# Kernel optimization log

Measured on AMD Instinct MI355X. Metric: run time of the kernel, lower is better.

## Reference

```python
import jax, jax.numpy as jnp
import numpy as np

B, T, DIM, H = 32, 1024, 512, 8
HD = DIM // H
HID = int(DIM * 4.0)
EPS = 1e-6
SCALE = HD ** -0.5


def _ln(t, g, b):
    m = t.mean(-1, keepdims=True)
    var = ((t - m) ** 2).mean(-1, keepdims=True)
    return (t - m) * jax.lax.rsqrt(var + EPS) * g + b


def setup_inputs() -> dict:
    key = jax.random.key(0)
    ks = jax.random.split(key, 10)
    n = lambda k, s: jax.random.normal(k, s, dtype=jnp.float32)
    w = lambda k, s: n(k, s) * 0.02
    z = lambda d: jnp.zeros((d,), dtype=jnp.float32)
    o = lambda d: jnp.ones((d,), dtype=jnp.float32)
    return {
        'x': n(ks[0], (B, T, DIM)),
        'k': n(ks[1], (T, H, B, HD)),
        'v': n(ks[2], (T, H, B, HD)),
        'Wqkv': w(ks[3], (DIM, 3 * DIM)), 'bqkv': z(3 * DIM),
        'Wsa': w(ks[4], (DIM, DIM)), 'bsa': z(DIM),
        'Wq': w(ks[5], (DIM, DIM)), 'bq': z(DIM),
        'Wed': w(ks[6], (DIM, DIM)), 'bed': z(DIM),
        'g1': o(DIM), 'be1': z(DIM),
        'g2': o(DIM), 'be2': z(DIM),
        'g3': o(DIM), 'be3': z(DIM),
        'W1': w(ks[7], (DIM, HID)), 'b1': z(HID),
        'W2': w(ks[8], (HID, DIM)), 'b2': z(DIM),
    }


def _decoder_block(x, k, v, Wqkv, bqkv, Wsa, bsa, Wq, bq, Wed, bed,
                   g1, be1, g2, be2, g3, be3, W1, b1, W2, b2):
    # ---- self-attention (faithful to the original, degenerate einsums) ----
    qkv = x @ Wqkv + bqkv                                        # [B,T,3*DIM]
    qkv = qkv.reshape(B, T, 3, H, HD).transpose(2, 1, 3, 0, 4)   # [3,T,H,B,HD]
    q, sk, sv = qkv[0], qkv[1], qkv[2]
    dp = jnp.einsum('kabc,qdef->qabe', sk, q) * SCALE            # [T,H,B,B]
    scores = jax.nn.softmax(dp, axis=-1)
    wa = jnp.einsum('qabc,kdef->bqaf', scores, sv).reshape(B, T, DIM)
    attn = wa @ Wsa + bsa
    an1 = _ln(attn + x, g1, be1)
    # ---- encoder-decoder attention ----
    qe = (an1 @ Wq + bq).reshape(B, T, H, HD).transpose(1, 2, 0, 3)  # [T,H,B,HD]
    dp2 = jnp.einsum('abkd,abqd->abqk', k, qe) * SCALE           # [T,H,B,B]
    sc2 = jax.nn.softmax(dp2, axis=-1)
    wa2 = jnp.einsum('abts,abse->tabe', sc2, v).reshape(B, T, DIM)
    attn2 = wa2 @ Wed + bed
    an2 = _ln(attn2 + x, g2, be2)
    # ---- MLP (exact GELU, as nn.GELU default) ----
    hmid = jax.nn.gelu(an2 @ W1 + b1, approximate=False)
    z = hmid @ W2 + b2
    return _ln(z + an2, g3, be3)


def reference(x, k, v, Wqkv, bqkv, Wsa, bsa, Wq, bq, Wed, bed,
              g1, be1, g2, be2, g3, be3, W1, b1, W2, b2):
    return _decoder_block(x, k, v, Wqkv, bqkv, Wsa, bsa, Wq, bq, Wed, bed,
                          g1, be1, g2, be2, g3, be3, W1, b1, W2, b2)
```

## Files before the change

kernel.cpp:

```cpp
#include <hip/hip_runtime.h>
#include <hip/hip_bf16.h>
#include <math.h>

#define Bn 32
#define Tn 1024
#define DIMn 512
#define Hn 8
#define HDn 64
#define HIDn 2048
#define Mn 32768

using short8 = __attribute__((ext_vector_type(8))) short;
using half8  = __attribute__((ext_vector_type(8))) _Float16;
using f32x4  = __attribute__((ext_vector_type(4))) float;
typedef unsigned short u16;
typedef unsigned int   u32;

__device__ __forceinline__ u16 f2h(float x) {
  _Float16 h = (_Float16)x;
  return __builtin_bit_cast(u16, h);
}
__device__ __forceinline__ float h2f(u16 u) {
  return (float)__builtin_bit_cast(_Float16, u);
}
__device__ __forceinline__ u32 pack2h(float a, float b) {
  return (u32)f2h(a) | ((u32)f2h(b) << 16);
}
__device__ __forceinline__ void gld16(const void* g, void* l) {
  __builtin_amdgcn_global_load_lds((const __attribute__((address_space(1))) u32*)g,
                                   (__attribute__((address_space(3))) u32*)l, 16, 0, 0);
}
__device__ __forceinline__ float wredsum(float v) {
  #pragma unroll
  for (int d = 1; d < 64; d <<= 1) v += __shfl_xor(v, d, 64);
  return v;
}
__device__ __forceinline__ void hard_barrier() {
  asm volatile("" ::: "memory");
  __builtin_amdgcn_s_barrier();
  asm volatile("" ::: "memory");
}
__device__ __forceinline__ float fast_gelu(float v) {
  const float ax = fabsf(v) * 0.70710678118654752f;
  const float t = 1.0f / (1.0f + 0.3275911f * ax);
  const float p = ((((1.061405429f * t - 1.453152027f) * t) + 1.421413741f) * t - 0.284496736f) * t + 0.254829592f;
  const float y = 1.0f - p * t * __expf(-ax * ax);
  const float erfv = (v >= 0.f) ? y : -y;
  return 0.5f * v * (1.0f + erfv);
}

__global__ __launch_bounds__(256) void colsum1(const float* __restrict__ x, float* __restrict__ part) {
  const int b = blockIdx.x, t = threadIdx.x;
  const float* p = x + (size_t)b * 128 * DIMn;
  float a0 = 0.f, a1 = 0.f;
  for (int r = 0; r < 128; ++r) {
    a0 += p[r * DIMn + t];
    a1 += p[r * DIMn + t + 256];
  }
  part[b * DIMn + t] = a0;
  part[b * DIMn + t + 256] = a1;
}

__global__ __launch_bounds__(256) void colsum2(const float* __restrict__ part, float* __restrict__ xs) {
  const int c = blockIdx.x * 256 + threadIdx.x;
  float a = 0.f;
  for (int b = 0; b < 256; ++b) a += part[b * DIMn + c];
  xs[c] = a;
}

__global__ __launch_bounds__(256) void sv_k(const float* __restrict__ xs, const float* __restrict__ Wqkv,
                                            const float* __restrict__ bqkv, float* __restrict__ SVp) {
  __shared__ float xsh[512];
  __shared__ float red[4][64];
  const int h = blockIdx.x, q = threadIdx.x >> 6, f = threadIdx.x & 63;
  xsh[threadIdx.x] = xs[threadIdx.x];
  xsh[threadIdx.x + 256] = xs[threadIdx.x + 256];
  __syncthreads();
  const int colb = 2 * DIMn + h * HDn + f;
  float acc = 0.f;
  for (int i = q * 128; i < q * 128 + 128; ++i) acc += xsh[i] * Wqkv[(size_t)i * 1536 + colb];
  red[q][f] = acc;
  __syncthreads();
  if (q == 0)
    SVp[h * 64 + f] = red[0][f] + red[1][f] + red[2][f] + red[3][f] + 32768.0f * bqkv[colb];
}

__global__ __launch_bounds__(256) void attnc2_k(const float* __restrict__ SVp, const float* __restrict__ Wsa,
                                                const float* __restrict__ bsa, float* __restrict__ attnc) {
  __shared__ float SVs[64];
  __shared__ float red[4][64];
  const int q = threadIdx.x >> 6, jj = threadIdx.x & 63;
  if (threadIdx.x < 64) {
    float s = 0.f;
    #pragma unroll
    for (int h = 0; h < 8; ++h) s += SVp[h * 64 + threadIdx.x];
    SVs[threadIdx.x] = s;
  }
  __syncthreads();
  const int j = blockIdx.x * 64 + jj;
  float acc = 0.f;
  for (int i = q * 128; i < q * 128 + 128; ++i) acc += SVs[i & 63] * Wsa[(size_t)i * DIMn + j];
  red[q][jj] = acc;
  __syncthreads();
  if (q == 0) attnc[j] = red[0][jj] + red[1][jj] + red[2][jj] + red[3][jj] + bsa[j];
}

__global__ __launch_bounds__(256) void wtrans(const float* __restrict__ W, u16* __restrict__ WT, int K, int N) {
  __shared__ float tile[64][65];
  const int n0 = blockIdx.x * 64, k0 = blockIdx.y * 64;
  const int t = threadIdx.x;
  #pragma unroll
  for (int i = 0; i < 16; ++i) {
    const int fl = i * 256 + t, r = fl >> 6, c = fl & 63;
    tile[r][c] = W[(size_t)(k0 + r) * N + n0 + c];
  }
  __syncthreads();
  #pragma unroll
  for (int i = 0; i < 16; ++i) {
    const int fl = i * 256 + t, r = fl >> 6, c = fl & 63;
    WT[(size_t)(n0 + r) * K + k0 + c] = f2h(tile[c][r]);
  }
}

template <int MODE>
__global__ __launch_bounds__(256) void ln_k(const void* __restrict__ Ap, const void* __restrict__ Bp,
                                            const float* __restrict__ cv, const float* __restrict__ g,
                                            const float* __restrict__ be, void* __restrict__ outp) {
  const int row = blockIdx.x * 4 + (threadIdx.x >> 6);
  const int l = threadIdx.x & 63;
  const size_t base = (size_t)row * DIMn + l * 8;
  float v[8];
  if (MODE == 0 || MODE == 2) {
    const float* a = (const float*)Ap + base;
    float4 x0 = *(const float4*)a;
    float4 x1 = *(const float4*)(a + 4);
    v[0] = x0.x; v[1] = x0.y; v[2] = x0.z; v[3] = x0.w;
    v[4] = x1.x; v[5] = x1.y; v[6] = x1.z; v[7] = x1.w;
  } else {
    short8 s = *(const short8*)((const u16*)Ap + base);
    #pragma unroll
    for (int i = 0; i < 8; ++i) v[i] = h2f((u16)s[i]);
  }
  if (MODE == 0) {
    float4 c0 = *(const float4*)(cv + l * 8);
    float4 c1 = *(const float4*)(cv + l * 8 + 4);
    v[0] += c0.x; v[1] += c0.y; v[2] += c0.z; v[3] += c0.w;
    v[4] += c1.x; v[5] += c1.y; v[6] += c1.z; v[7] += c1.w;
  } else if (MODE == 1) {
    const float* b = (const float*)Bp + base;
    float4 x0 = *(const float4*)b;
    float4 x1 = *(const float4*)(b + 4);
    v[0] += x0.x; v[1] += x0.y; v[2] += x0.z; v[3] += x0.w;
    v[4] += x1.x; v[5] += x1.y; v[6] += x1.z; v[7] += x1.w;
  } else {
    short8 s2 = *(const short8*)((const u16*)Bp + base);
    #pragma unroll
    for (int i = 0; i < 8; ++i) v[i] += h2f((u16)s2[i]);
  }
  float s = 0.f;
  #pragma unroll
  for (int i = 0; i < 8; ++i) s += v[i];
  s = wredsum(s);
  const float mean = s * (1.0f / 512.0f);
  float q = 0.f;
  #pragma unroll
  for (int i = 0; i < 8; ++i) { const float d = v[i] - mean; q += d * d; }
  q = wredsum(q);
  const float rs = rsqrtf(q * (1.0f / 512.0f) + 1e-6f);
  float gg[8], bb[8];
  {
    float4 g0 = *(const float4*)(g + l * 8);
    float4 g1 = *(const float4*)(g + l * 8 + 4);
    float4 b0 = *(const float4*)(be + l * 8);
    float4 b1 = *(const float4*)(be + l * 8 + 4);
    gg[0] = g0.x; gg[1] = g0.y; gg[2] = g0.z; gg[3] = g0.w;
    gg[4] = g1.x; gg[5] = g1.y; gg[6] = g1.z; gg[7] = g1.w;
    bb[0] = b0.x; bb[1] = b0.y; bb[2] = b0.z; bb[3] = b0.w;
    bb[4] = b1.x; bb[5] = b1.y; bb[6] = b1.z; bb[7] = b1.w;
  }
  float y[8];
  #pragma unroll
  for (int i = 0; i < 8; ++i) y[i] = (v[i] - mean) * rs * gg[i] + bb[i];
  if (MODE == 2) {
    float* o = (float*)outp + base;
    *(float4*)o = make_float4(y[0], y[1], y[2], y[3]);
    *(float4*)(o + 4) = make_float4(y[4], y[5], y[6], y[7]);
  } else {
    short8 o;
    #pragma unroll
    for (int i = 0; i < 8; ++i) o[i] = (short)f2h(y[i]);
    *(short8*)((u16*)outp + base) = o;
  }
}

#define CPAD 132
template <bool GELU, bool OBF>
__global__ __launch_bounds__(256) void gemm128(const u16* __restrict__ A, const u16* __restrict__ BT,
                                               const float* __restrict__ bias, u16* __restrict__ OB,
                                               float* __restrict__ OF, int Ni, int Ki, int gridX) {
  __shared__ u16 smem[3 * 8192];
  const int tid = threadIdx.x;
  const int l = tid & 63, w = tid >> 6, wr = w >> 1, wc = w & 1;

  int wg = blockIdx.x;
  const int nwg = gridDim.x;
  if ((nwg & 7) == 0) {
    const int q = nwg >> 3;
    wg = (wg & 7) * q + (wg >> 3);
  }
  const int bx = wg % gridX, by = wg / gridX;
  const int m0 = by * 128, n0 = bx * 128;
  const int r16 = l & 15, g4 = l >> 4;

  const int schunk = (tid & 3) ^ ((tid >> 2) & 3);
  const u16* ga = A + (size_t)(m0 + (tid >> 2)) * (size_t)Ki + schunk * 8;
  const u16* gb = BT + (size_t)(n0 + (tid >> 2)) * (size_t)Ki + schunk * 8;
  const int ldst = tid * 8;

  const int g4s = g4 ^ (r16 & 3);
  int aoff[4], boff[4];
  #pragma unroll
  for (int i = 0; i < 4; ++i) {
    aoff[i] = (wr * 64 + i * 16 + r16) * 32 + g4s * 8;
    boff[i] = 4096 + (wc * 64 + i * 16 + r16) * 32 + g4s * 8;
  }
  f32x4 acc[4][4] = {};

  const int nt = Ki >> 5;
  auto STAGE = [&](int t, int b) {
    u16* base = smem + b * 8192;
    const int kk = t * 32;
    gld16(ga + kk, &base[ldst]);
    gld16(ga + kk + (size_t)64 * Ki, &base[ldst + 2048]);
    gld16(gb + kk, &base[4096 + ldst]);
    gld16(gb + kk + (size_t)64 * Ki, &base[4096 + ldst + 2048]);
  };

  STAGE(0, 0);
  STAGE(1, 1);
  int b0 = 0, b1 = 1, b2 = 2;
  for (int t = 0; t < nt; ++t) {
    if (t < nt - 1) asm volatile("s_waitcnt vmcnt(4)" ::: "memory");
    else            asm volatile("s_waitcnt vmcnt(0)" ::: "memory");
    hard_barrier();
    if (t + 2 < nt) STAGE(t + 2, b2);
    const u16* base = smem + b0 * 8192;
    half8 af[4], bf[4];
    #pragma unroll
    for (int i = 0; i < 4; ++i) af[i] = *(const half8*)&base[aoff[i]];
    #pragma unroll
    for (int i = 0; i < 4; ++i) bf[i] = *(const half8*)&base[boff[i]];
    #pragma unroll
    for (int mi = 0; mi < 4; ++mi)
      #pragma unroll
      for (int ni = 0; ni < 4; ++ni)
        acc[mi][ni] = __builtin_amdgcn_mfma_f32_16x16x32_f16(af[mi], bf[ni], acc[mi][ni], 0, 0, 0);
    hard_barrier();
    const int tb = b0; b0 = b1; b1 = b2; b2 = tb;
  }

  if (OBF) {
    u16* Cs = smem;
    #pragma unroll
    for (int ni = 0; ni < 4; ++ni) {
      const int col = wc * 64 + ni * 16 + r16;
      const float bv = bias[n0 + col];
      #pragma unroll
      for (int mi = 0; mi < 4; ++mi) {
        const int rowb = wr * 64 + mi * 16 + g4 * 4;
        #pragma unroll
        for (int r = 0; r < 4; ++r) {
          float v = acc[mi][ni][r] + bv;
          if (GELU) v = fast_gelu(v);
          Cs[(rowb + r) * CPAD + col] = f2h(v);
        }
      }
    }
    hard_barrier();
    const int rr = tid >> 4;
    const int c0 = (tid & 15) * 8;
    #pragma unroll
    for (int j = 0; j < 8; ++j) {
      const int row = rr + j * 16;
      *(short8*)(OB + (size_t)(m0 + row) * Ni + n0 + c0) = *(const short8*)&Cs[row * CPAD + c0];
    }
  } else {
    #pragma unroll
    for (int ni = 0; ni < 4; ++ni) {
      const int col = n0 + wc * 64 + ni * 16 + r16;
      const float bv = bias[col];
      #pragma unroll
      for (int mi = 0; mi < 4; ++mi) {
        const int rowb = m0 + wr * 64 + mi * 16 + g4 * 4;
        #pragma unroll
        for (int r = 0; r < 4; ++r) {
          float v = acc[mi][ni][r] + bv;
          if (GELU) v = fast_gelu(v);
          OF[(size_t)(rowb + r) * Ni + col] = v;
        }
      }
    }
  }
}

#define CROW 272
template <bool GELU, bool OBF>
__global__ __launch_bounds__(512) void gemm256(const u16* __restrict__ A, const u16* __restrict__ BT,
                                               const float* __restrict__ bias, u16* __restrict__ OB,
                                               float* __restrict__ OF, int Ni, int Ki, int gridX) {
  __shared__ u16 smem[49152];
  const int tid = threadIdx.x;
  const int l = tid & 63, wid = tid >> 6, wr = wid >> 2, wc = wid & 3;

  int wg = blockIdx.x;
  const int nwg = gridDim.x;
  if ((nwg & 7) == 0) {
    const int q = nwg >> 3;
    wg = (wg & 7) * q + (wg >> 3);
  }
  const int bx = wg % gridX, by = wg / gridX;
  const int m0 = by * 256, n0 = bx * 256;
  const int r16 = l & 15, g4 = l >> 4;

  const int srow = tid >> 2, schunk = (tid & 3) * 8;
  const u16* gaA = A  + (size_t)(m0 + srow) * (size_t)Ki + schunk;
  const u16* gaB = BT + (size_t)(n0 + srow) * (size_t)Ki + schunk;
  const size_t rowskip = (size_t)128 * (size_t)Ki;
  const int ldst = tid * 8;

  int aoff[8], boff[4];
  #pragma unroll
  for (int mi = 0; mi < 8; ++mi) aoff[mi] = (wr * 128 + mi * 16 + r16) * 32 + g4 * 8;
  #pragma unroll
  for (int ni = 0; ni < 4; ++ni) boff[ni] = 8192 + (wc * 64 + ni * 16 + r16) * 32 + g4 * 8;

  f32x4 acc[8][4] = {};
  const int nt = Ki >> 5;

  auto STAGE = [&](int t, int b) {
    u16* base = smem + b * 16384;
    const int kk = t * 32;
    gld16(gaA + kk, &base[ldst]);
    gld16(gaA + kk + rowskip, &base[ldst + 4096]);
    gld16(gaB + kk, &base[8192 + ldst]);
    gld16(gaB + kk + rowskip, &base[8192 + ldst + 4096]);
  };

  STAGE(0, 0);
  STAGE(1, 1);
  int b0 = 0, b1 = 1, b2 = 2;
  for (int t = 0; t < nt; ++t) {
    if (t < nt - 1) asm volatile("s_waitcnt vmcnt(4)" ::: "memory");
    else            asm volatile("s_waitcnt vmcnt(0)" ::: "memory");
    hard_barrier();
    if (t + 2 < nt) STAGE(t + 2, b2);
    const u16* base = smem + b0 * 16384;
    half8 bf[4];
    #pragma unroll
    for (int ni = 0; ni < 4; ++ni) bf[ni] = *(const half8*)&base[boff[ni]];
    #pragma unroll
    for (int mi = 0; mi < 8; ++mi) {
      half8 af = *(const half8*)&base[aoff[mi]];
      #pragma unroll
      for (int ni = 0; ni < 4; ++ni)
        acc[mi][ni] = __builtin_amdgcn_mfma_f32_16x16x32_f16(af, bf[ni], acc[mi][ni], 0, 0, 0);
    }
    hard_barrier();
    const int tb = b0; b0 = b1; b1 = b2; b2 = tb;
  }

  if (OBF) {
    u16* Cs = smem;
    float bv[4];
    #pragma unroll
    for (int ni = 0; ni < 4; ++ni) bv[ni] = bias[n0 + wc * 64 + ni * 16 + r16];
    #pragma unroll
    for (int p = 0; p < 2; ++p) {
      #pragma unroll
      for (int mi4 = 0; mi4 < 4; ++mi4) {
        const int mi = p * 4 + mi4;
        #pragma unroll
        for (int ni = 0; ni < 4; ++ni) {
          const int colL = wc * 64 + ni * 16 + r16;
          #pragma unroll
          for (int r = 0; r < 4; ++r) {
            float v = acc[mi][ni][r] + bv[ni];
            if (GELU) v = fast_gelu(v);
            Cs[wr * (64 * CROW) + (mi4 * 16 + g4 * 4 + r) * CROW + colL] = f2h(v);
          }
        }
      }
      hard_barrier();
      #pragma unroll
      for (int j = 0; j < 8; ++j) {
        const int s = tid + j * 512;
        const int wrS = s >> 11;
        const int rowL = (s & 2047) >> 5;
        const int c8 = s & 31;
        *(short8*)(OB + (size_t)(m0 + wrS * 128 + p * 64 + rowL) * Ni + n0 + c8 * 8) =
            *(const short8*)&Cs[wrS * (64 * CROW) + rowL * CROW + c8 * 8];
      }
      if (p == 0) hard_barrier();
    }
  } else {
    #pragma unroll
    for (int ni = 0; ni < 4; ++ni) {
      const int col = n0 + wc * 64 + ni * 16 + r16;
      const float bvv = bias[col];
      #pragma unroll
      for (int mi = 0; mi < 8; ++mi) {
        const int rowb = m0 + wr * 128 + mi * 16 + g4 * 4;
        #pragma unroll
        for (int r = 0; r < 4; ++r) {
          float v = acc[mi][ni][r] + bvv;
          if (GELU) v = fast_gelu(v);
          OF[(size_t)(rowb + r) * Ni + col] = v;
        }
      }
    }
  }
}

template <bool RESF32, bool OUTF32>
__global__ __launch_bounds__(512) void gemm_fln(const u16* __restrict__ A, const u16* __restrict__ BT,
                                                const float* __restrict__ bias, const void* __restrict__ resid,
                                                const float* __restrict__ g, const float* __restrict__ be,
                                                void* __restrict__ out, int Ki) {
  __shared__ u16 smem[61440];
  const int tid = threadIdx.x;
  const int l = tid & 63, wid = tid >> 6, wr = wid >> 2, wc = wid & 3;
  const int m0 = blockIdx.x * 128;
  const int r16 = l & 15, g4 = l >> 4;

  const u16* gA = A  + (size_t)(m0 + (tid >> 2)) * (size_t)Ki + (tid & 3) * 8;
  const u16* gB = BT + (size_t)(tid >> 2) * (size_t)Ki + (tid & 3) * 8;
  const size_t r128 = (size_t)128 * Ki;

  int aoff[4], boff[8];
  #pragma unroll
  for (int mi = 0; mi < 4; ++mi) aoff[mi] = (wr * 64 + mi * 16 + r16) * 32 + g4 * 8;
  #pragma unroll
  for (int ni = 0; ni < 8; ++ni) boff[ni] = 4096 + (wc * 128 + ni * 16 + r16) * 32 + g4 * 8;

  f32x4 acc[4][8] = {};
  const int nt = Ki >> 5;

  auto STAGE = [&](int t, int b) {
    u16* base = smem + b * 20480;
    const int kk = t * 32;
    gld16(gA + kk, &base[tid * 8]);
    #pragma unroll
    for (int j = 0; j < 4; ++j)
      gld16(gB + kk + (size_t)j * r128, &base[4096 + tid * 8 + j * 4096]);
  };

  STAGE(0, 0);
  STAGE(1, 1);
  int b0 = 0, b1 = 1, b2 = 2;
  for (int t = 0; t < nt; ++t) {
    if (t < nt - 1) asm volatile("s_waitcnt vmcnt(5)" ::: "memory");
    else            asm volatile("s_waitcnt vmcnt(0)" ::: "memory");
    hard_barrier();
    if (t + 2 < nt) STAGE(t + 2, b2);
    const u16* base = smem + b0 * 20480;
    half8 af[4];
    #pragma unroll
    for (int mi = 0; mi < 4; ++mi) af[mi] = *(const half8*)&base[aoff[mi]];
    #pragma unroll
    for (int ni = 0; ni < 8; ++ni) {
      half8 bf = *(const half8*)&base[boff[ni]];
      #pragma unroll
      for (int mi = 0; mi < 4; ++mi)
        acc[mi][ni] = __builtin_amdgcn_mfma_f32_16x16x32_f16(af[mi], bf, acc[mi][ni], 0, 0, 0);
    }
    hard_barrier();
    const int tb = b0; b0 = b1; b1 = b2; b2 = tb;
  }

  float* Ls = (float*)smem;
  float bv[8];
  #pragma unroll
  for (int ni = 0; ni < 8; ++ni) bv[ni] = bias[wc * 128 + ni * 16 + r16];
  #pragma unroll
  for (int rg = 0; rg < 4; ++rg) {
    if (wr == (rg >> 1)) {
      #pragma unroll
      for (int mi2 = 0; mi2 < 2; ++mi2) {
        const int mi = (rg & 1) * 2 + mi2;
        #pragma unroll
        for (int ni = 0; ni < 8; ++ni) {
          const int col = wc * 128 + ni * 16 + r16;
          #pragma unroll
          for (int r = 0; r < 4; ++r)
            Ls[(mi2 * 16 + g4 * 4 + r) * 516 + col] = acc[mi][ni][r] + bv[ni];
        }
      }
    }
    hard_barrier();
    #pragma unroll
    for (int pass = 0; pass < 4; ++pass) {
      const int rl = pass * 8 + wid;
      const size_t grow = (size_t)(m0 + rg * 32 + rl);
      float v[8];
      if (RESF32) {
        const float* rp = (const float*)resid + grow * DIMn + l * 8;
        float4 x0 = *(const float4*)rp;
        float4 x1 = *(const float4*)(rp + 4);
        v[0] = Ls[rl * 516 + l * 8 + 0] + x0.x; v[1] = Ls[rl * 516 + l * 8 + 1] + x0.y;
        v[2] = Ls[rl * 516 + l * 8 + 2] + x0.z; v[3] = Ls[rl * 516 + l * 8 + 3] + x0.w;
        v[4] = Ls[rl * 516 + l * 8 + 4] + x1.x; v[5] = Ls[rl * 516 + l * 8 + 5] + x1.y;
        v[6] = Ls[rl * 516 + l * 8 + 6] + x1.z; v[7] = Ls[rl * 516 + l * 8 + 7] + x1.w;
      } else {
        short8 s2 = *(const short8*)((const u16*)resid + grow * DIMn + l * 8);
        #pragma unroll
        for (int i = 0; i < 8; ++i) v[i] = Ls[rl * 516 + l * 8 + i] + h2f((u16)s2[i]);
      }
      float s = 0.f;
      #pragma unroll
      for (int i = 0; i < 8; ++i) s += v[i];
      s = wredsum(s);
      const float mean = s * (1.0f / 512.0f);
      float q = 0.f;
      #pragma unroll
      for (int i = 0; i < 8; ++i) { const float d = v[i] - mean; q += d * d; }
      q = wredsum(q);
      const float rs = rsqrtf(q * (1.0f / 512.0f) + 1e-6f);
      float4 g0 = *(const float4*)(g + l * 8);
      float4 g1 = *(const float4*)(g + l * 8 + 4);
      float4 e0 = *(const float4*)(be + l * 8);
      float4 e1 = *(const float4*)(be + l * 8 + 4);
      float y[8];
      y[0] = (v[0] - mean) * rs * g0.x + e0.x; y[1] = (v[1] - mean) * rs * g0.y + e0.y;
      y[2] = (v[2] - mean) * rs * g0.z + e0.z; y[3] = (v[3] - mean) * rs * g0.w + e0.w;
      y[4] = (v[4] - mean) * rs * g1.x + e1.x; y[5] = (v[5] - mean) * rs * g1.y + e1.y;
      y[6] = (v[6] - mean) * rs * g1.z + e1.z; y[7] = (v[7] - mean) * rs * g1.w + e1.w;
      if (OUTF32) {
        float* o = (float*)out + grow * DIMn + l * 8;
        *(float4*)o = make_float4(y[0], y[1], y[2], y[3]);
        *(float4*)(o + 4) = make_float4(y[4], y[5], y[6], y[7]);
      } else {
        short8 o;
        #pragma unroll
        for (int i = 0; i < 8; ++i) o[i] = (short)f2h(y[i]);
        *(short8*)((u16*)out + grow * DIMn + l * 8) = o;
      }
    }
    hard_barrier();
  }
}

__global__ __launch_bounds__(64) void attn_k(const u16* __restrict__ qe, const float* __restrict__ kin,
                                             const float* __restrict__ vin, u16* __restrict__ wa2) {
  const int t = blockIdx.x >> 3;
  const int h = blockIdx.x & 7;
  const int l = threadIdx.x;
  __shared__ u16 Kq[32 * 80];
  __shared__ u16 Qq[32 * 80];
  __shared__ u16 VT[64 * 48];
  __shared__ u16 Ps[32 * 48];

  const float* kp = kin + (size_t)blockIdx.x * 2048;
  const float* vp = vin + (size_t)blockIdx.x * 2048;
  #pragma unroll
  for (int i = 0; i < 8; ++i) {
    const int fl = i * 256 + l * 4;
    const int r = fl >> 6, c = fl & 63;
    float4 kv = *(const float4*)(kp + fl);
    float4 vv = *(const float4*)(vp + fl);
    *(u32*)&Kq[r * 80 + c]     = pack2h(kv.x, kv.y);
    *(u32*)&Kq[r * 80 + c + 2] = pack2h(kv.z, kv.w);
    VT[(c + 0) * 48 + r] = f2h(vv.x);
    VT[(c + 1) * 48 + r] = f2h(vv.y);
    VT[(c + 2) * 48 + r] = f2h(vv.z);
    VT[(c + 3) * 48 + r] = f2h(vv.w);
  }
  {
    const int qb = l >> 1, hf = l & 1;
    const u16* qp = qe + (size_t)(qb * Tn + t) * DIMn + h * HDn + hf * 32;
    #pragma unroll
    for (int j = 0; j < 4; ++j) {
      short8 d = *(const short8*)(qp + j * 8);
      *(short8*)&Qq[qb * 80 + hf * 32 + j * 8] = d;
    }
  }
  __syncthreads();

  const int r16 = l & 15, g4 = l >> 4;
  f32x4 sacc[2][2] = {};
  #pragma unroll
  for (int kk = 0; kk < 2; ++kk) {
    half8 aQ0 = *(const half8*)&Qq[r16 * 80 + kk * 32 + g4 * 8];
    half8 aQ1 = *(const half8*)&Qq[(16 + r16) * 80 + kk * 32 + g4 * 8];
    half8 bK0 = *(const half8*)&Kq[r16 * 80 + kk * 32 + g4 * 8];
    half8 bK1 = *(const half8*)&Kq[(16 + r16) * 80 + kk * 32 + g4 * 8];
    sacc[0][0] = __builtin_amdgcn_mfma_f32_16x16x32_f16(aQ0, bK0, sacc[0][0], 0, 0, 0);
    sacc[0][1] = __builtin_amdgcn_mfma_f32_16x16x32_f16(aQ0, bK1, sacc[0][1], 0, 0, 0);
    sacc[1][0] = __builtin_amdgcn_mfma_f32_16x16x32_f16(aQ1, bK0, sacc[1][0], 0, 0, 0);
    sacc[1][1] = __builtin_amdgcn_mfma_f32_16x16x32_f16(aQ1, bK1, sacc[1][1], 0, 0, 0);
  }
  #pragma unroll
  for (int m = 0; m < 2; ++m) {
    #pragma unroll
    for (int r = 0; r < 4; ++r) {
      const float a0 = sacc[m][0][r] * 0.125f;
      const float a1 = sacc[m][1][r] * 0.125f;
      float mx = fmaxf(a0, a1);
      #pragma unroll
      for (int d = 1; d < 16; d <<= 1) mx = fmaxf(mx, __shfl_xor(mx, d, 64));
      const float e0 = __expf(a0 - mx), e1 = __expf(a1 - mx);
      float sm = e0 + e1;
      #pragma unroll
      for (int d = 1; d < 16; d <<= 1) sm += __shfl_xor(sm, d, 64);
      const float inv = 1.0f / sm;
      const int rr = m * 16 + g4 * 4 + r;
      Ps[rr * 48 + r16]      = f2h(e0 * inv);
      Ps[rr * 48 + 16 + r16] = f2h(e1 * inv);
    }
  }
  __syncthreads();

  half8 aP0 = *(const half8*)&Ps[r16 * 48 + g4 * 8];
  half8 aP1 = *(const half8*)&Ps[(16 + r16) * 48 + g4 * 8];
  f32x4 oacc[2][4] = {};
  #pragma unroll
  for (int nn = 0; nn < 4; ++nn) {
    half8 bV = *(const half8*)&VT[(nn * 16 + r16) * 48 + g4 * 8];
    oacc[0][nn] = __builtin_amdgcn_mfma_f32_16x16x32_f16(aP0, bV, oacc[0][nn], 0, 0, 0);
    oacc[1][nn] = __builtin_amdgcn_mfma_f32_16x16x32_f16(aP1, bV, oacc[1][nn], 0, 0, 0);
  }
  #pragma unroll
  for (int m = 0; m < 2; ++m) {
    #pragma unroll
    for (int r = 0; r < 4; ++r) {
      const int qb = m * 16 + g4 * 4 + r;
      u16* op = wa2 + (size_t)(qb * Tn + t) * DIMn + h * HDn;
      #pragma unroll
      for (int nn = 0; nn < 4; ++nn)
        op[nn * 16 + r16] = f2h(oacc[m][nn][r]);
    }
  }
}

extern "C" void kernel_launch(void* const* d_in, const int* in_sizes, int n_in,
                              void* d_out, int out_size, void* d_ws, size_t ws_size,
                              hipStream_t stream) {
  (void)in_sizes; (void)n_in; (void)out_size;
  const float* x    = (const float*)d_in[0];
  const float* kin  = (const float*)d_in[1];
  const float* vin  = (const float*)d_in[2];
  const float* Wqkv = (const float*)d_in[3];
  const float* bqkv = (const float*)d_in[4];
  const float* Wsa  = (const float*)d_in[5];
  const float* bsa  = (const float*)d_in[6];
  const float* Wq   = (const float*)d_in[7];
  const float* bq   = (const float*)d_in[8];
  const float* Wed  = (const float*)d_in[9];
  const float* bed  = (const float*)d_in[10];
  const float* g1   = (const float*)d_in[11];
  const float* be1  = (const float*)d_in[12];
  const float* g2   = (const float*)d_in[13];
  const float* be2  = (const float*)d_in[14];
  const float* g3   = (const float*)d_in[15];
  const float* be3  = (const float*)d_in[16];
  const float* W1   = (const float*)d_in[17];
  const float* b1   = (const float*)d_in[18];
  const float* W2   = (const float*)d_in[19];
  const float* b2   = (const float*)d_in[20];

  char* ws = (char*)d_ws;
  float* xs    = (float*)(ws);
  float* SVp   = (float*)(ws + (2 << 10));
  float* attnc = (float*)(ws + (4 << 10));
  float* part  = (float*)(ws + (6 << 10));
  u16* wqT  = (u16*)(ws + (1 << 20));
  u16* wedT = (u16*)(ws + (1 << 20) + (512 << 10));
  u16* w1T  = (u16*)(ws + (2 << 20));
  u16* w2T  = (u16*)(ws + (4 << 20));
  u16* Abuf = (u16*)(ws + (6 << 20));
  const size_t HOFF = 38ull << 20;
  u16* hmid = (u16*)(ws + HOFF);

  u16* an1  = Abuf;
  u16* wa2  = Abuf;
  u16* an2b = Abuf;
  u16*   qe   = (u16*)d_out;
  float* outf = (float*)d_out;

  long long avail = (long long)ws_size - (long long)HOFF;
  int crows = (avail > 0) ? (int)(avail / (HIDn * 2)) : 256;
  crows = (crows / 256) * 256;
  if (crows < 256) crows = 256;
  if (crows > Mn) crows = Mn;

  colsum1<<<256, 256, 0, stream>>>(x, part);
  colsum2<<<2, 256, 0, stream>>>(part, xs);
  sv_k<<<8, 256, 0, stream>>>(xs, Wqkv, bqkv, SVp);
  attnc2_k<<<8, 256, 0, stream>>>(SVp, Wsa, bsa, attnc);

  wtrans<<<dim3(8, 8),  256, 0, stream>>>(Wq,  wqT,  512, 512);
  wtrans<<<dim3(8, 8),  256, 0, stream>>>(Wed, wedT, 512, 512);
  wtrans<<<dim3(32, 8), 256, 0, stream>>>(W1,  w1T,  512, 2048);
  wtrans<<<dim3(8, 32), 256, 0, stream>>>(W2,  w2T,  2048, 512);

  ln_k<0><<<Mn / 4, 256, 0, stream>>>(x, nullptr, attnc, g1, be1, an1);
  gemm256<false, true><<<256, 512, 0, stream>>>(an1, wqT, bq, qe, nullptr, 512, 512, 2);
  attn_k<<<Tn * Hn, 64, 0, stream>>>(qe, kin, vin, wa2);
  gemm_fln<true, false><<<Mn / 128, 512, 0, stream>>>(wa2, wedT, bed, x, g2, be2, an2b, 512);
  for (int r0 = 0; r0 < Mn; r0 += crows) {
    int rc = Mn - r0; if (rc > crows) rc = crows;
    gemm128<true, true><<<16 * (rc / 128), 256, 0, stream>>>(an2b + (size_t)r0 * DIMn, w1T, b1, hmid, nullptr, HIDn, DIMn, 16);
    gemm_fln<false, true><<<rc / 128, 512, 0, stream>>>(hmid, w2T, b2, an2b + (size_t)r0 * DIMn, g3, be3,
                                                        outf + (size_t)r0 * DIMn, HIDn);
  }
}
```

Before: 389.2 us.

## Replace gemm128/gemm256 with a wide 128x512-tile GEMM for Wq and W1

Replaces the two GEMM kernels with one 512-thread kernel that computes a 128x512 output tile. Each workgroup streams the A rows once per 512 columns, which is meant to cut A re-reads and give more MFMA work per LDS load. It is used for the Wq projection and the GELU W1 GEMM. The change drops the LDS XOR swizzle the old 128 kernel had, uses 120KB of LDS, and writes the epilogue through LDS in 32-row groups with extra barriers. The risks are bank conflicts, lower occupancy, and a smaller grid for the Wq GEMM.

```diff
diff --git a/kernel.cpp b/kernel.cpp
--- a/kernel.cpp
+++ b/kernel.cpp
@@ -193,14 +193,13 @@
   }
 }
 
-#define CPAD 132
-template <bool GELU, bool OBF>
-__global__ __launch_bounds__(256) void gemm128(const u16* __restrict__ A, const u16* __restrict__ BT,
+template <bool GELU>
+__global__ __launch_bounds__(512) void gemm_fw(const u16* __restrict__ A, const u16* __restrict__ BT,
                                                const float* __restrict__ bias, u16* __restrict__ OB,
-                                               float* __restrict__ OF, int Ni, int Ki, int gridX) {
-  __shared__ u16 smem[3 * 8192];
+                                               int Ki, int NB) {
+  __shared__ u16 smem[61440];
   const int tid = threadIdx.x;
-  const int l = tid & 63, w = tid >> 6, wr = w >> 1, wc = w & 1;
+  const int l = tid & 63, wid = tid >> 6, wr = wid >> 2, wc = wid & 3;
 
   int wg = blockIdx.x;
   const int nwg = gridDim.x;
@@ -208,216 +207,87 @@
     const int q = nwg >> 3;
     wg = (wg & 7) * q + (wg >> 3);
   }
-  const int bx = wg % gridX, by = wg / gridX;
-  const int m0 = by * 128, n0 = bx * 128;
+  const int mb = wg / NB, nb = wg % NB;
+  const int m0 = mb * 128, n0 = nb * 512;
+  const int Nfull = NB * 512;
   const int r16 = l & 15, g4 = l >> 4;
 
-  const int schunk = (tid & 3) ^ ((tid >> 2) & 3);
-  const u16* ga = A + (size_t)(m0 + (tid >> 2)) * (size_t)Ki + schunk * 8;
-  const u16* gb = BT + (size_t)(n0 + (tid >> 2)) * (size_t)Ki + schunk * 8;
-  const int ldst = tid * 8;
-
-  const int g4s = g4 ^ (r16 & 3);
-  int aoff[4], boff[4];
-  #pragma unroll
-  for (int i = 0; i < 4; ++i) {
-    aoff[i] = (wr * 64 + i * 16 + r16) * 32 + g4s * 8;
-    boff[i] = 4096 + (wc * 64 + i * 16 + r16) * 32 + g4s * 8;
-  }
-  f32x4 acc[4][4] = {};
-
+  const u16* gA = A  + (size_t)(m0 + (tid >> 2)) * (size_t)Ki + (tid & 3) * 8;
+  const u16* gB = BT + (size_t)(n0 + (tid >> 2)) * (size_t)Ki + (tid & 3) * 8;
+  const size_t r128 = (size_t)128 * Ki;
+
+  int aoff[4], boff[8];
+  #pragma unroll
+  for (int mi = 0; mi < 4; ++mi) aoff[mi] = (wr * 64 + mi * 16 + r16) * 32 + g4 * 8;
+  #pragma unroll
+  for (int ni = 0; ni < 8; ++ni) boff[ni] = 4096 + (wc * 128 + ni * 16 + r16) * 32 + g4 * 8;
+
+  f32x4 acc[4][8] = {};
   const int nt = Ki >> 5;
+
   auto STAGE = [&](int t, int b) {
-    u16* base = smem + b * 8192;
+    u16* base = smem + b * 20480;
     const int kk = t * 32;
-    gld16(ga + kk, &base[ldst]);
-    gld16(ga + kk + (size_t)64 * Ki, &base[ldst + 2048]);
-    gld16(gb + kk, &base[4096 + ldst]);
-    gld16(gb + kk + (size_t)64 * Ki, &base[4096 + ldst + 2048]);
+    gld16(gA + kk, &base[tid * 8]);
+    #pragma unroll
+    for (int j = 0; j < 4; ++j)
+      gld16(gB + kk + (size_t)j * r128, &base[4096 + tid * 8 + j * 4096]);
   };
 
   STAGE(0, 0);
   STAGE(1, 1);
   int b0 = 0, b1 = 1, b2 = 2;
   for (int t = 0; t < nt; ++t) {
-    if (t < nt - 1) asm volatile("s_waitcnt vmcnt(4)" ::: "memory");
+    if (t < nt - 1) asm volatile("s_waitcnt vmcnt(5)" ::: "memory");
     else            asm volatile("s_waitcnt vmcnt(0)" ::: "memory");
     hard_barrier();
     if (t + 2 < nt) STAGE(t + 2, b2);
-    const u16* base = smem + b0 * 8192;
-    half8 af[4], bf[4];
-    #pragma unroll
-    for (int i = 0; i < 4; ++i) af[i] = *(const half8*)&base[aoff[i]];
-    #pragma unroll
-    for (int i = 0; i < 4; ++i) bf[i] = *(const half8*)&base[boff[i]];
-    #pragma unroll
-    for (int mi = 0; mi < 4; ++mi)
-      #pragma unroll
-      for (int ni = 0; ni < 4; ++ni)
-        acc[mi][ni] = __builtin_amdgcn_mfma_f32_16x16x32_f16(af[mi], bf[ni], acc[mi][ni], 0, 0, 0);
+    const u16* base = smem + b0 * 20480;
+    half8 af[4];
+    #pragma unroll
+    for (int mi = 0; mi < 4; ++mi) af[mi] = *(const half8*)&base[aoff[mi]];
+    #pragma unroll
+    for (int ni = 0; ni < 8; ++ni) {
+      half8 bf = *(const half8*)&base[boff[ni]];
+      #pragma unroll
+      for (int mi = 0; mi < 4; ++mi)
+        acc[mi][ni] = __builtin_amdgcn_mfma_f32_16x16x32_f16(af[mi], bf, acc[mi][ni], 0, 0, 0);
+    }
     hard_barrier();
     const int tb = b0; b0 = b1; b1 = b2; b2 = tb;
   }
 
-  if (OBF) {
-    u16* Cs = smem;
-    #pragma unroll
-    for (int ni = 0; ni < 4; ++ni) {
-      const int col = wc * 64 + ni * 16 + r16;
-      const float bv = bias[n0 + col];
-      #pragma unroll
-      for (int mi = 0; mi < 4; ++mi) {
-        const int rowb = wr * 64 + mi * 16 + g4 * 4;
+  u16* Ls = smem;
+  float bv[8];
+  #pragma unroll
+  for (int ni = 0; ni < 8; ++ni) bv[ni] = bias[n0 + wc * 128 + ni * 16 + r16];
+  #pragma unroll
+  for (int rg = 0; rg < 4; ++rg) {
+    if (wr == (rg >> 1)) {
+      #pragma unroll
+      for (int mi2 = 0; mi2 < 2; ++mi2) {
+        const int mi = (rg & 1) * 2 + mi2;
         #pragma unroll
-        for (int r = 0; r < 4; ++r) {
-          float v = acc[mi][ni][r] + bv;
-          if (GELU) v = fast_gelu(v);
-          Cs[(rowb + r) * CPAD + col] = f2h(v);
-        }
-      }
-    }
-    hard_barrier();
-    const int rr = tid >> 4;
-    const int c0 = (tid & 15) * 8;
-    #pragma unroll
-    for (int j = 0; j < 8; ++j) {
-      const int row = rr + j * 16;
-      *(short8*)(OB + (size_t)(m0 + row) * Ni + n0 + c0) = *(const short8*)&Cs[row * CPAD + c0];
-    }
-  } else {
-    #pragma unroll
-    for (int ni = 0; ni < 4; ++ni) {
-      const int col = n0 + wc * 64 + ni * 16 + r16;
-      const float bv = bias[col];
-      #pragma unroll
-      for (int mi = 0; mi < 4; ++mi) {
-        const int rowb = m0 + wr * 64 + mi * 16 + g4 * 4;
-        #pragma unroll
-        for (int r = 0; r < 4; ++r) {
-          float v = acc[mi][ni][r] + bv;
-          if (GELU) v = fast_gelu(v);
-          OF[(size_t)(rowb + r) * Ni + col] = v;
-        }
-      }
-    }
-  }
-}
-
-#define CROW 272
-template <bool GELU, bool OBF>
-__global__ __launch_bounds__(512) void gemm256(const u16* __restrict__ A, const u16* __restrict__ BT,
-                                               const float* __restrict__ bias, u16* __restrict__ OB,
-                                               float* __restrict__ OF, int Ni, int Ki, int gridX) {
-  __shared__ u16 smem[49152];
-  const int tid = threadIdx.x;
-  const int l = tid & 63, wid = tid >> 6, wr = wid >> 2, wc = wid & 3;
-
-  int wg = blockIdx.x;
-  const int nwg = gridDim.x;
-  if ((nwg & 7) == 0) {
-    const int q = nwg >> 3;
-    wg = (wg & 7) * q + (wg >> 3);
-  }
-  const int bx = wg % gridX, by = wg / gridX;
-  const int m0 = by * 256, n0 = bx * 256;
-  const int r16 = l & 15, g4 = l >> 4;
-
-  const int srow = tid >> 2, schunk = (tid & 3) * 8;
-  const u16* gaA = A  + (size_t)(m0 + srow) * (size_t)Ki + schunk;
-  const u16* gaB = BT + (size_t)(n0 + srow) * (size_t)Ki + schunk;
-  const size_t rowskip = (size_t)128 * (size_t)Ki;
-  const int ldst = tid * 8;
-
-  int aoff[8], boff[4];
-  #pragma unroll
-  for (int mi = 0; mi < 8; ++mi) aoff[mi] = (wr * 128 + mi * 16 + r16) * 32 + g4 * 8;
-  #pragma unroll
-  for (int ni = 0; ni < 4; ++ni) boff[ni] = 8192 + (wc * 64 + ni * 16 + r16) * 32 + g4 * 8;
-
-  f32x4 acc[8][4] = {};
-  const int nt = Ki >> 5;
-
-  auto STAGE = [&](int t, int b) {
-    u16* base = smem + b * 16384;
-    const int kk = t * 32;
-    gld16(gaA + kk, &base[ldst]);
-    gld16(gaA + kk + rowskip, &base[ldst + 4096]);
-    gld16(gaB + kk, &base[8192 + ldst]);
-    gld16(gaB + kk + rowskip, &base[8192 + ldst + 4096]);
-  };
-
-  STAGE(0, 0);
-  STAGE(1, 1);
-  int b0 = 0, b1 = 1, b2 = 2;
-  for (int t = 0; t < nt; ++t) {
-    if (t < nt - 1) asm volatile("s_waitcnt vmcnt(4)" ::: "memory");
-    else            asm volatile("s_waitcnt vmcnt(0)" ::: "memory");
-    hard_barrier();
-    if (t + 2 < nt) STAGE(t + 2, b2);
-    const u16* base = smem + b0 * 16384;
-    half8 bf[4];
-    #pragma unroll
-    for (int ni = 0; ni < 4; ++ni) bf[ni] = *(const half8*)&base[boff[ni]];
-    #pragma unroll
-    for (int mi = 0; mi < 8; ++mi) {
-      half8 af = *(const half8*)&base[aoff[mi]];
-      #pragma unroll
-      for (int ni = 0; ni < 4; ++ni)
-        acc[mi][ni] = __builtin_amdgcn_mfma_f32_16x16x32_f16(af, bf[ni], acc[mi][ni], 0, 0, 0);
-    }
-    hard_barrier();
-    const int tb = b0; b0 = b1; b1 = b2; b2 = tb;
-  }
-
-  if (OBF) {
-    u16* Cs = smem;
-    float bv[4];
-    #pragma unroll
-    for (int ni = 0; ni < 4; ++ni) bv[ni] = bias[n0 + wc * 64 + ni * 16 + r16];
-    #pragma unroll
-    for (int p = 0; p < 2; ++p) {
-      #pragma unroll
-      for (int mi4 = 0; mi4 < 4; ++mi4) {
-        const int mi = p * 4 + mi4;
-        #pragma unroll
-        for (int ni = 0; ni < 4; ++ni) {
-          const int colL = wc * 64 + ni * 16 + r16;
+        for (int ni = 0; ni < 8; ++ni) {
+          const int col = wc * 128 + ni * 16 + r16;
           #pragma unroll
           for (int r = 0; r < 4; ++r) {
             float v = acc[mi][ni][r] + bv[ni];
             if (GELU) v = fast_gelu(v);
-            Cs[wr * (64 * CROW) + (mi4 * 16 + g4 * 4 + r) * CROW + colL] = f2h(v);
+            Ls[(mi2 * 16 + g4 * 4 + r) * 520 + col] = f2h(v);
           }
         }
       }
-      hard_barrier();
-      #pragma unroll
-      for (int j = 0; j < 8; ++j) {
-        const int s = tid + j * 512;
-        const int wrS = s >> 11;
-        const int rowL = (s & 2047) >> 5;
-        const int c8 = s & 31;
-        *(short8*)(OB + (size_t)(m0 + wrS * 128 + p * 64 + rowL) * Ni + n0 + c8 * 8) =
-            *(const short8*)&Cs[wrS * (64 * CROW) + rowL * CROW + c8 * 8];
-      }
-      if (p == 0) hard_barrier();
-    }
-  } else {
-    #pragma unroll
-    for (int ni = 0; ni < 4; ++ni) {
-      const int col = n0 + wc * 64 + ni * 16 + r16;
-      const float bvv = bias[col];
-      #pragma unroll
-      for (int mi = 0; mi < 8; ++mi) {
-        const int rowb = m0 + wr * 128 + mi * 16 + g4 * 4;
-        #pragma unroll
-        for (int r = 0; r < 4; ++r) {
-          float v = acc[mi][ni][r] + bvv;
-          if (GELU) v = fast_gelu(v);
-          OF[(size_t)(rowb + r) * Ni + col] = v;
-        }
-      }
-    }
+    }
+    hard_barrier();
+    #pragma unroll
+    for (int pass = 0; pass < 4; ++pass) {
+      const int rl = pass * 8 + wid;
+      const size_t grow = (size_t)(m0 + rg * 32 + rl);
+      short8 o = *(const short8*)&Ls[rl * 520 + l * 8];
+      *(short8*)(OB + grow * (size_t)Nfull + n0 + l * 8) = o;
+    }
+    hard_barrier();
   }
 }
 
@@ -703,12 +573,12 @@
   wtrans<<<dim3(8, 32), 256, 0, stream>>>(W2,  w2T,  2048, 512);
 
   ln_k<0><<<Mn / 4, 256, 0, stream>>>(x, nullptr, attnc, g1, be1, an1);
-  gemm256<false, true><<<256, 512, 0, stream>>>(an1, wqT, bq, qe, nullptr, 512, 512, 2);
+  gemm_fw<false><<<Mn / 128, 512, 0, stream>>>(an1, wqT, bq, qe, 512, 1);
   attn_k<<<Tn * Hn, 64, 0, stream>>>(qe, kin, vin, wa2);
   gemm_fln<true, false><<<Mn / 128, 512, 0, stream>>>(wa2, wedT, bed, x, g2, be2, an2b, 512);
   for (int r0 = 0; r0 < Mn; r0 += crows) {
     int rc = Mn - r0; if (rc > crows) rc = crows;
-    gemm128<true, true><<<16 * (rc / 128), 256, 0, stream>>>(an2b + (size_t)r0 * DIMn, w1T, b1, hmid, nullptr, HIDn, DIMn, 16);
+    gemm_fw<true><<<(rc / 128) * 4, 512, 0, stream>>>(an2b + (size_t)r0 * DIMn, w1T, b1, hmid, DIMn, 4);
     gemm_fln<false, true><<<rc / 128, 512, 0, stream>>>(hmid, w2T, b2, an2b + (size_t)r0 * DIMn, g3, be3,
                                                         outf + (size_t)r0 * DIMn, HIDn);
   }
```

Result: slower. 582.7 us (+49.7%).

## Replace 128x128 W1 GEMM with 128x512-tile 512-thread kernel

Applied to the files above, without the earlier changes.

The first MLP GEMM (W1 + GELU) moves from a 256-thread 128x128-tile kernel with a 3-stage pipeline to a new 512-thread kernel using 128x512 tiles and a 2-stage double buffer. Each A tile is reused across four times as many output columns, which cuts redundant A reads and raises MFMA work per loaded byte. The trade-offs are more accumulator registers per thread (4x8 f32x4), which may lower occupancy, fewer workgroups per chunk, a shallower pipeline, and an LDS row layout with no XOR swizzle that can cause bank conflicts. The epilogue stages output through LDS in 32-row slices for coalesced stores.

```diff
diff --git a/kernel.cpp b/kernel.cpp
--- a/kernel.cpp
+++ b/kernel.cpp
@@ -193,116 +193,6 @@
   }
 }
 
-#define CPAD 132
-template <bool GELU, bool OBF>
-__global__ __launch_bounds__(256) void gemm128(const u16* __restrict__ A, const u16* __restrict__ BT,
-                                               const float* __restrict__ bias, u16* __restrict__ OB,
-                                               float* __restrict__ OF, int Ni, int Ki, int gridX) {
-  __shared__ u16 smem[3 * 8192];
-  const int tid = threadIdx.x;
-  const int l = tid & 63, w = tid >> 6, wr = w >> 1, wc = w & 1;
-
-  int wg = blockIdx.x;
-  const int nwg = gridDim.x;
-  if ((nwg & 7) == 0) {
-    const int q = nwg >> 3;
-    wg = (wg & 7) * q + (wg >> 3);
-  }
-  const int bx = wg % gridX, by = wg / gridX;
-  const int m0 = by * 128, n0 = bx * 128;
-  const int r16 = l & 15, g4 = l >> 4;
-
-  const int schunk = (tid & 3) ^ ((tid >> 2) & 3);
-  const u16* ga = A + (size_t)(m0 + (tid >> 2)) * (size_t)Ki + schunk * 8;
-  const u16* gb = BT + (size_t)(n0 + (tid >> 2)) * (size_t)Ki + schunk * 8;
-  const int ldst = tid * 8;
-
-  const int g4s = g4 ^ (r16 & 3);
-  int aoff[4], boff[4];
-  #pragma unroll
-  for (int i = 0; i < 4; ++i) {
-    aoff[i] = (wr * 64 + i * 16 + r16) * 32 + g4s * 8;
-    boff[i] = 4096 + (wc * 64 + i * 16 + r16) * 32 + g4s * 8;
-  }
-  f32x4 acc[4][4] = {};
-
-  const int nt = Ki >> 5;
-  auto STAGE = [&](int t, int b) {
-    u16* base = smem + b * 8192;
-    const int kk = t * 32;
-    gld16(ga + kk, &base[ldst]);
-    gld16(ga + kk + (size_t)64 * Ki, &base[ldst + 2048]);
-    gld16(gb + kk, &base[4096 + ldst]);
-    gld16(gb + kk + (size_t)64 * Ki, &base[4096 + ldst + 2048]);
-  };
-
-  STAGE(0, 0);
-  STAGE(1, 1);
-  int b0 = 0, b1 = 1, b2 = 2;
-  for (int t = 0; t < nt; ++t) {
-    if (t < nt - 1) asm volatile("s_waitcnt vmcnt(4)" ::: "memory");
-    else            asm volatile("s_waitcnt vmcnt(0)" ::: "memory");
-    hard_barrier();
-    if (t + 2 < nt) STAGE(t + 2, b2);
-    const u16* base = smem + b0 * 8192;
-    half8 af[4], bf[4];
-    #pragma unroll
-    for (int i = 0; i < 4; ++i) af[i] = *(const half8*)&base[aoff[i]];
-    #pragma unroll
-    for (int i = 0; i < 4; ++i) bf[i] = *(const half8*)&base[boff[i]];
-    #pragma unroll
-    for (int mi = 0; mi < 4; ++mi)
-      #pragma unroll
-      for (int ni = 0; ni < 4; ++ni)
-        acc[mi][ni] = __builtin_amdgcn_mfma_f32_16x16x32_f16(af[mi], bf[ni], acc[mi][ni], 0, 0, 0);
-    hard_barrier();
-    const int tb = b0; b0 = b1; b1 = b2; b2 = tb;
-  }
-
-  if (OBF) {
-    u16* Cs = smem;
-    #pragma unroll
-    for (int ni = 0; ni < 4; ++ni) {
-      const int col = wc * 64 + ni * 16 + r16;
-      const float bv = bias[n0 + col];
-      #pragma unroll
-      for (int mi = 0; mi < 4; ++mi) {
-        const int rowb = wr * 64 + mi * 16 + g4 * 4;
-        #pragma unroll
-        for (int r = 0; r < 4; ++r) {
-          float v = acc[mi][ni][r] + bv;
-          if (GELU) v = fast_gelu(v);
-          Cs[(rowb + r) * CPAD + col] = f2h(v);
-        }
-      }
-    }
-    hard_barrier();
-    const int rr = tid >> 4;
-    const int c0 = (tid & 15) * 8;
-    #pragma unroll
-    for (int j = 0; j < 8; ++j) {
-      const int row = rr + j * 16;
-      *(short8*)(OB + (size_t)(m0 + row) * Ni + n0 + c0) = *(const short8*)&Cs[row * CPAD + c0];
-    }
-  } else {
-    #pragma unroll
-    for (int ni = 0; ni < 4; ++ni) {
-      const int col = n0 + wc * 64 + ni * 16 + r16;
-      const float bv = bias[col];
-      #pragma unroll
-      for (int mi = 0; mi < 4; ++mi) {
-        const int rowb = m0 + wr * 64 + mi * 16 + g4 * 4;
-        #pragma unroll
-        for (int r = 0; r < 4; ++r) {
-          float v = acc[mi][ni][r] + bv;
-          if (GELU) v = fast_gelu(v);
-          OF[(size_t)(rowb + r) * Ni + col] = v;
-        }
-      }
-    }
-  }
-}
-
 #define CROW 272
 template <bool GELU, bool OBF>
 __global__ __launch_bounds__(512) void gemm256(const u16* __restrict__ A, const u16* __restrict__ BT,
@@ -418,6 +308,104 @@
         }
       }
     }
+  }
+}
+
+template <bool GELU>
+__global__ __launch_bounds__(512) void gemm_fwB(const u16* __restrict__ A, const u16* __restrict__ BT,
+                                                const float* __restrict__ bias, u16* __restrict__ OB,
+                                                int Ki, int NB) {
+  __shared__ u16 smem[40960];
+  const int tid = threadIdx.x;
+  const int l = tid & 63, wid = tid >> 6, wr = wid >> 2, wc = wid & 3;
+
+  int wg = blockIdx.x;
+  const int nwg = gridDim.x;
+  if ((nwg & 7) == 0) {
+    const int q = nwg >> 3;
+    wg = (wg & 7) * q + (wg >> 3);
+  }
+  const int mb = wg / NB, nb = wg % NB;
+  const int m0 = mb * 128, n0 = nb * 512;
+  const int Nfull = NB * 512;
+  const int r16 = l & 15, g4 = l >> 4;
+
+  const u16* gA = A  + (size_t)(m0 + (tid >> 2)) * (size_t)Ki + (tid & 3) * 8;
+  const u16* gB = BT + (size_t)(n0 + (tid >> 2)) * (size_t)Ki + (tid & 3) * 8;
+  const size_t r128 = (size_t)128 * Ki;
+
+  int aoff[4], boff[8];
+  #pragma unroll
+  for (int mi = 0; mi < 4; ++mi) aoff[mi] = (wr * 64 + mi * 16 + r16) * 32 + g4 * 8;
+  #pragma unroll
+  for (int ni = 0; ni < 8; ++ni) boff[ni] = 4096 + (wc * 128 + ni * 16 + r16) * 32 + g4 * 8;
+
+  f32x4 acc[4][8] = {};
+  const int nt = Ki >> 5;
+
+  auto STAGE = [&](int t, int b) {
+    u16* base = smem + b * 20480;
+    const int kk = t * 32;
+    gld16(gA + kk, &base[tid * 8]);
+    #pragma unroll
+    for (int j = 0; j < 4; ++j)
+      gld16(gB + kk + (size_t)j * r128, &base[4096 + tid * 8 + j * 4096]);
+  };
+
+  STAGE(0, 0);
+  for (int t = 0; t < nt; ++t) {
+    if (t + 1 < nt) {
+      STAGE(t + 1, (t + 1) & 1);
+      asm volatile("s_waitcnt vmcnt(5)" ::: "memory");
+    } else {
+      asm volatile("s_waitcnt vmcnt(0)" ::: "memory");
+    }
+    hard_barrier();
+    const u16* base = smem + (t & 1) * 20480;
+    half8 af[4];
+    #pragma unroll
+    for (int mi = 0; mi < 4; ++mi) af[mi] = *(const half8*)&base[aoff[mi]];
+    #pragma unroll
+    for (int ni = 0; ni < 8; ++ni) {
+      half8 bf = *(const half8*)&base[boff[ni]];
+      #pragma unroll
+      for (int mi = 0; mi < 4; ++mi)
+        acc[mi][ni] = __builtin_amdgcn_mfma_f32_16x16x32_f16(af[mi], bf, acc[mi][ni], 0, 0, 0);
+    }
+    hard_barrier();
+  }
+
+  u16* Ls = smem;
+  float bv[8];
+  #pragma unroll
+  for (int ni = 0; ni < 8; ++ni) bv[ni] = bias[n0 + wc * 128 + ni * 16 + r16];
+  #pragma unroll
+  for (int rg = 0; rg < 4; ++rg) {
+    if (wr == (rg >> 1)) {
+      #pragma unroll
+      for (int mi2 = 0; mi2 < 2; ++mi2) {
+        const int mi = (rg & 1) * 2 + mi2;
+        #pragma unroll
+        for (int ni = 0; ni < 8; ++ni) {
+          const int col = wc * 128 + ni * 16 + r16;
+          #pragma unroll
+          for (int r = 0; r < 4; ++r) {
+            float v = acc[mi][ni][r] + bv[ni];
+            if (GELU) v = fast_gelu(v);
+            Ls[(mi2 * 16 + g4 * 4 + r) * 520 + col] = f2h(v);
+          }
+        }
+      }
+    }
+    hard_barrier();
+    #pragma unroll
+    for (int pass = 0; pass < 4; ++pass) {
+      const int rl = pass * 8 + wid;
+      const size_t grow = (size_t)(m0 + rg * 32 + rl);
+      short8 o = *(const short8*)&Ls[rl * 520 + l * 8];
+      *(short8*)(OB + grow * (size_t)Nfull + n0 + l * 8) = o;
+    }
+    hard_barrier();
   }
 }
 
@@ -708,7 +696,7 @@
   gemm_fln<true, false><<<Mn / 128, 512, 0, stream>>>(wa2, wedT, bed, x, g2, be2, an2b, 512);
   for (int r0 = 0; r0 < Mn; r0 += crows) {
     int rc = Mn - r0; if (rc > crows) rc = crows;
-    gemm128<true, true><<<16 * (rc / 128), 256, 0, stream>>>(an2b + (size_t)r0 * DIMn, w1T, b1, hmid, nullptr, HIDn, DIMn, 16);
+    gemm_fwB<true><<<(rc / 128) * 4, 512, 0, stream>>>(an2b + (size_t)r0 * DIMn, w1T, b1, hmid, DIMn, 4);
     gemm_fln<false, true><<<rc / 128, 512, 0, stream>>>(hmid, w2T, b2, an2b + (size_t)r0 * DIMn, g3, be3,
                                                         outf + (size_t)r0 * DIMn, HIDn);
   }
```

After: 593.8 us. 52.6% more time.
